# Kernel optimization log

Measured on AMD Instinct MI355X. Metric: run time of the kernel, lower is better.

Reference implementation:

```python
import jax, jax.numpy as jnp
import numpy as np

N_NODES = 50000
N_EDGES = 800000
D_IN, D_HID, D_OUT = 128, 128, 64


def setup_inputs() -> dict:
    key = jax.random.key(0)
    ks = jax.random.split(key, 8)
    x = jax.random.normal(ks[0], (N_NODES, D_IN), dtype=jnp.float32)
    edge_index = jax.random.randint(ks[1], (2, N_EDGES), 0, N_NODES, dtype=jnp.int64)

    def glorot(k, shape):
        fan_in, fan_out = shape
        lim = jnp.sqrt(6.0 / (fan_in + fan_out)).astype(jnp.float32)
        return jax.random.uniform(k, shape, jnp.float32, -lim, lim)

    return {
        "x": x,
        "edge_index": edge_index,
        "W1": glorot(ks[2], (D_IN, D_HID)),
        "b1": jnp.zeros((D_HID,), jnp.float32),
        "W2": glorot(ks[3], (D_HID, D_HID)),
        "b2": jnp.zeros((D_HID,), jnp.float32),
        "W3": glorot(ks[4], (D_HID, D_OUT)),
        "b3": jnp.zeros((D_OUT,), jnp.float32),
    }


def reference(x, edge_index, W1, b1, W2, b2, W3, b3):
    # PyG GCNConv with normalize=False: h = x @ W, then sum-aggregate source
    # features onto targets (edge_index[0]=src, edge_index[1]=dst), add bias.
    src = edge_index[0]
    dst = edge_index[1]
    n = x.shape[0]

    def gcn_layer(h, W, b):
        hw = h @ W                      # [N, d_out] dense GEMM
        msg = hw[src]                   # [E, d_out] gather
        agg = jax.ops.segment_sum(msg, dst, num_segments=n)  # [N, d_out] scatter-add
        return agg + b

    o1 = gcn_layer(x, W1, b1)
    o2 = gcn_layer(o1, W2, b2)
    o3 = gcn_layer(o2, W3, b3)
    return (o1, o2, o3)
```

## Files before the change

kernel.cpp:

```cpp
#include <hip/hip_runtime.h>

#define N_NODES 50000
#define N_EDGES 800000
#define CAP 64

typedef unsigned int uint32;
typedef unsigned short u16;

typedef __attribute__((ext_vector_type(8))) short bf16x8;
typedef __attribute__((ext_vector_type(4))) float f32x4;

__device__ __forceinline__ uint32 f32_to_bf16_rne(float f) {
    uint32 u = __float_as_uint(f);
    u += 0x7fffu + ((u >> 16) & 1u);
    return u >> 16;
}
__device__ __forceinline__ float bf16lo_to_f32(uint32 v) { return __uint_as_float(v << 16); }
__device__ __forceinline__ float bf16hi_to_f32(uint32 v) { return __uint_as_float(v & 0xffff0000u); }

__global__ __launch_bounds__(256) void prep_kernel(const float* __restrict__ W1,
                                                   const float* __restrict__ W2,
                                                   const float* __restrict__ W3,
                                                   uint32* __restrict__ wt1,
                                                   uint32* __restrict__ wt2,
                                                   uint32* __restrict__ wt3,
                                                   int* __restrict__ cursor) {
    int b = blockIdx.x, tid = threadIdx.x;
    if (b < 196) {
        int i = b * 256 + tid;
        if (i < N_NODES) cursor[i] = 0;
        return;
    }
    b -= 196;
    const float* W;
    uint32* WT;
    int N;
    if (b < 32) { W = W1; WT = wt1; N = 128; }
    else if (b < 64) { W = W2; WT = wt2; N = 128; b -= 32; }
    else { W = W3; WT = wt3; N = 64; b -= 64; }
    int i = b * 256 + tid;
    if (i >= N * 64) return;
    int n = i >> 6, p = i & 63;
    WT[n * 64 + p] = f32_to_bf16_rne(W[(2 * p) * N + n]) |
                     (f32_to_bf16_rne(W[(2 * p + 1) * N + n]) << 16);
}

__device__ __forceinline__ void gather_pair(const uint32* __restrict__ hwb,
                                            int myslot, int d, int lane,
                                            float& ax, float& ay, float& az, float& aw) {
    const int h = lane >> 5;
    const int li = lane & 31;
    int e = 0;
    for (; e + 16 <= d; e += 16) {
        uint2 v[8];
#pragma unroll
        for (int j = 0; j < 8; j++) {
            int s = __shfl(myslot, e + 2 * j + h);
            v[j] = *reinterpret_cast<const uint2*>(&hwb[(size_t)s * 64 + li * 2]);
        }
#pragma unroll
        for (int j = 0; j < 8; j++) {
            ax += bf16lo_to_f32(v[j].x); ay += bf16hi_to_f32(v[j].x);
            az += bf16lo_to_f32(v[j].y); aw += bf16hi_to_f32(v[j].y);
        }
    }
    for (; e < d; e += 2) {
        int idx = e + h;
        int s = __shfl(myslot, idx < d ? idx : e);
        uint2 v = make_uint2(0u, 0u);
        if (idx < d) v = *reinterpret_cast<const uint2*>(&hwb[(size_t)s * 64 + li * 2]);
        ax += bf16lo_to_f32(v.x); ay += bf16hi_to_f32(v.x);
        az += bf16lo_to_f32(v.y); aw += bf16hi_to_f32(v.y);
    }
    ax += __shfl_xor(ax, 32);
    ay += __shfl_xor(ay, 32);
    az += __shfl_xor(az, 32);
    aw += __shfl_xor(aw, 32);
}

__device__ __forceinline__ void pack_store(uint32* __restrict__ Cb, int rowstride_u,
                                           int row, int col, int r16, float v) {
    float nb = __shfl_xor(v, 1);
    if ((r16 & 1) == 0) {
        uint32 p = f32_to_bf16_rne(v) | (f32_to_bf16_rne(nb) << 16);
        Cb[(size_t)row * rowstride_u + (col >> 1)] = p;
    }
}

__device__ __forceinline__ void gemm1_body(const float* __restrict__ A,
                                           const uint32* __restrict__ WTb,
                                           uint32* __restrict__ Cb, int M, int bid) {
    constexpr int NT = 2;
    const int tid = threadIdx.x;
    const int wave = tid >> 6;
    const int lane = tid & 63;
    const int r16 = lane & 15;
    const int g = lane >> 4;
    const int row0 = bid * 64;

    const float4* A4 = reinterpret_cast<const float4*>(A);
    const uint4* B4 = reinterpret_cast<const uint4*>(WTb);

    f32x4 acc[4][NT];
#pragma unroll
    for (int m = 0; m < 4; m++)
#pragma unroll
        for (int nt = 0; nt < NT; nt++) acc[m][nt] = (f32x4){0.f, 0.f, 0.f, 0.f};

    int rowm[4];
#pragma unroll
    for (int m = 0; m < 4; m++) {
        int r = row0 + m * 16 + r16;
        rowm[m] = r < M ? r : M - 1;
    }
    union U { uint4 u; bf16x8 v; };
#pragma unroll
    for (int kt = 0; kt < 4; kt++) {
        U b[NT];
#pragma unroll
        for (int nt = 0; nt < NT; nt++)
            b[nt].u = B4[(size_t)(nt * 64 + wave * 16 + r16) * 16 + kt * 4 + g];
        U a[4];
#pragma unroll
        for (int m = 0; m < 4; m++) {
            float4 f0 = A4[(size_t)rowm[m] * 32 + kt * 8 + g * 2];
            float4 f1 = A4[(size_t)rowm[m] * 32 + kt * 8 + g * 2 + 1];
            a[m].u.x = f32_to_bf16_rne(f0.x) | (f32_to_bf16_rne(f0.y) << 16);
            a[m].u.y = f32_to_bf16_rne(f0.z) | (f32_to_bf16_rne(f0.w) << 16);
            a[m].u.z = f32_to_bf16_rne(f1.x) | (f32_to_bf16_rne(f1.y) << 16);
            a[m].u.w = f32_to_bf16_rne(f1.z) | (f32_to_bf16_rne(f1.w) << 16);
        }
#pragma unroll
        for (int m = 0; m < 4; m++)
#pragma unroll
            for (int nt = 0; nt < NT; nt++)
                acc[m][nt] = __builtin_amdgcn_mfma_f32_16x16x32_bf16(a[m].v, b[nt].v, acc[m][nt], 0, 0, 0);
    }
#pragma unroll
    for (int m = 0; m < 4; m++)
#pragma unroll
        for (int nt = 0; nt < NT; nt++)
#pragma unroll
            for (int r = 0; r < 4; r++) {
                int row = row0 + m * 16 + g * 4 + r;
                if (row < M)
                    pack_store(Cb, 64, row, nt * 64 + wave * 16 + r16, r16, acc[m][nt][r]);
            }
}

#define EPT 8
#define EPB (256 * EPT)
#define GEMM1_BLOCKS 782
#define BUILD_CHUNKS 391

__global__ __launch_bounds__(256) void build_gemm1_kernel(const float* __restrict__ x,
                                                          const uint32* __restrict__ wt1,
                                                          uint32* __restrict__ hwb,
                                                          const int* __restrict__ ei,
                                                          int* __restrict__ cursor,
                                                          u16* __restrict__ adj) {
    if (blockIdx.x < GEMM1_BLOCKS) {
        gemm1_body(x, wt1, hwb, N_NODES, blockIdx.x);
        return;
    }
    const int bb = blockIdx.x - GEMM1_BLOCKS;
    const int part = bb & 7;
    const int chunk = bb >> 3;
    const int base = chunk * EPB + threadIdx.x * EPT;
#pragma unroll
    for (int i = 0; i < EPT; i += 4) {
        int e = base + i;
        if (e + 3 < N_EDGES) {
            int4 s4 = *reinterpret_cast<const int4*>(&ei[e]);
            int4 d4 = *reinterpret_cast<const int4*>(&ei[N_EDGES + e]);
            int ss[4] = {s4.x, s4.y, s4.z, s4.w};
            int dd[4] = {d4.x, d4.y, d4.z, d4.w};
#pragma unroll
            for (int j = 0; j < 4; j++) {
                int d = dd[j];
                if (((d >> 4) & 7) == part && (unsigned)d < (unsigned)N_NODES) {
                    int s = ss[j];
                    if ((unsigned)s >= (unsigned)N_NODES) s = 0;
                    int pos = atomicAdd(&cursor[d], 1);
                    if (pos < CAP) adj[d * CAP + pos] = (u16)s;
                }
            }
        } else {
            for (int j = 0; j < 4; j++) {
                int ee = e + j;
                if (ee < N_EDGES) {
                    int d = ei[N_EDGES + ee];
                    if (((d >> 4) & 7) == part && (unsigned)d < (unsigned)N_NODES) {
                        int s = ei[ee];
                        if ((unsigned)s >= (unsigned)N_NODES) s = 0;
                        int pos = atomicAdd(&cursor[d], 1);
                        if (pos < CAP) adj[d * CAP + pos] = (u16)s;
                    }
                }
            }
        }
    }
}

template <int N>
__global__ __launch_bounds__(256) void agg_gemm_kernel(const uint32* __restrict__ hw_in,
                                                       const u16* __restrict__ adj,
                                                       const int* __restrict__ deg,
                                                       const float* __restrict__ bias,
                                                       float* __restrict__ o_out,
                                                       const uint32* __restrict__ WTb,
                                                       uint32* __restrict__ hw_out) {
    constexpr int TPW = N / 64;
    constexpr int LDR = 68;
    __shared__ uint32 Asm[16 * LDR];

    const int tid = threadIdx.x;
    const int wave = tid >> 6;
    const int lane = tid & 63;
    const int li = lane & 31;
    const int base = blockIdx.x * 16;
    const float4* bias4 = reinterpret_cast<const float4*>(bias);

#pragma unroll
    for (int i = 0; i < 4; i++) {
        int n = base + wave * 4 + i;
        int d = __builtin_amdgcn_readfirstlane(deg[n]);
        if (d > CAP) d = CAP;
        int myslot = adj[n * CAP + lane];
        float ax = 0.f, ay = 0.f, az = 0.f, aw = 0.f;
        gather_pair(hw_in, myslot, d, lane, ax, ay, az, aw);
        if (lane < 32) {
            float4 b = bias4[li];
            ax += b.x; ay += b.y; az += b.z; aw += b.w;
            *reinterpret_cast<float4*>(&o_out[(size_t)n * 128 + li * 4]) =
                make_float4(ax, ay, az, aw);
            uint2 p;
            p.x = f32_to_bf16_rne(ax) | (f32_to_bf16_rne(ay) << 16);
            p.y = f32_to_bf16_rne(az) | (f32_to_bf16_rne(aw) << 16);
            *reinterpret_cast<uint2*>(&Asm[(wave * 4 + i) * LDR + li * 2]) = p;
        }
    }
    __syncthreads();

    const int r16 = lane & 15;
    const int g = lane >> 4;
    const uint4* B4 = reinterpret_cast<const uint4*>(WTb);

    f32x4 acc[TPW];
#pragma unroll
    for (int nt = 0; nt < TPW; nt++) acc[nt] = (f32x4){0.f, 0.f, 0.f, 0.f};

    union U { uint4 u; bf16x8 v; };
#pragma unroll
    for (int kt = 0; kt < 4; kt++) {
        U a;
        a.u = *reinterpret_cast<const uint4*>(&Asm[r16 * LDR + (kt * 4 + g) * 4]);
        U b[TPW];
#pragma unroll
        for (int nt = 0; nt < TPW; nt++) {
            int col = (wave * TPW + nt) * 16 + r16;
            b[nt].u = B4[(size_t)col * 16 + kt * 4 + g];
        }
#pragma unroll
        for (int nt = 0; nt < TPW; nt++)
            acc[nt] = __builtin_amdgcn_mfma_f32_16x16x32_bf16(a.v, b[nt].v, acc[nt], 0, 0, 0);
    }
#pragma unroll
    for (int nt = 0; nt < TPW; nt++)
#pragma unroll
        for (int r = 0; r < 4; r++) {
            int row = base + g * 4 + r;
            pack_store(hw_out, N / 2, row, (wave * TPW + nt) * 16 + r16, r16, acc[nt][r]);
        }
}

__global__ __launch_bounds__(256) void aggregate64_kernel(const uint32* __restrict__ hwb,
                                                          const u16* __restrict__ adj,
                                                          const int* __restrict__ deg,
                                                          const float* __restrict__ bias,
                                                          float* __restrict__ out) {
    int n = (blockIdx.x * blockDim.x + threadIdx.x) >> 6;
    if (n >= N_NODES) return;
    const int lane = threadIdx.x & 63;
    const int q = lane >> 4;
    const int li = lane & 15;
    int d = __builtin_amdgcn_readfirstlane(deg[n]);
    if (d > CAP) d = CAP;
    int myslot = adj[n * CAP + lane];

    float ax = 0.f, ay = 0.f, az = 0.f, aw = 0.f;
    int e = 0;
    for (; e + 32 <= d; e += 32) {
        uint2 v[8];
#pragma unroll
        for (int j = 0; j < 8; j++) {
            int s = __shfl(myslot, e + 4 * j + q);
            v[j] = *reinterpret_cast<const uint2*>(&hwb[(size_t)s * 32 + li * 2]);
        }
#pragma unroll
        for (int j = 0; j < 8; j++) {
            ax += bf16lo_to_f32(v[j].x); ay += bf16hi_to_f32(v[j].x);
            az += bf16lo_to_f32(v[j].y); aw += bf16hi_to_f32(v[j].y);
        }
    }
    for (; e < d; e += 4) {
        int idx = e + q;
        int s = __shfl(myslot, idx < d ? idx : e);
        uint2 v = make_uint2(0u, 0u);
        if (idx < d) v = *reinterpret_cast<const uint2*>(&hwb[(size_t)s * 32 + li * 2]);
        ax += bf16lo_to_f32(v.x); ay += bf16hi_to_f32(v.x);
        az += bf16lo_to_f32(v.y); aw += bf16hi_to_f32(v.y);
    }
    ax += __shfl_xor(ax, 32); ay += __shfl_xor(ay, 32);
    az += __shfl_xor(az, 32); aw += __shfl_xor(aw, 32);
    ax += __shfl_xor(ax, 16); ay += __shfl_xor(ay, 16);
    az += __shfl_xor(az, 16); aw += __shfl_xor(aw, 16);
    if (lane < 16) {
        const float4* bias4 = reinterpret_cast<const float4*>(bias);
        float4 b = bias4[li];
        *reinterpret_cast<float4*>(&out[(size_t)n * 64 + li * 4]) =
            make_float4(ax + b.x, ay + b.y, az + b.z, aw + b.w);
    }
}

extern "C" void kernel_launch(void* const* d_in, const int* in_sizes, int n_in,
                              void* d_out, int out_size, void* d_ws, size_t ws_size,
                              hipStream_t stream) {
    const float* x  = (const float*)d_in[0];
    const int*   ei = (const int*)d_in[1];
    const float* W1 = (const float*)d_in[2];
    const float* b1 = (const float*)d_in[3];
    const float* W2 = (const float*)d_in[4];
    const float* b2 = (const float*)d_in[5];
    const float* W3 = (const float*)d_in[6];
    const float* b3 = (const float*)d_in[7];

    float* o1 = (float*)d_out;
    float* o2 = o1 + (size_t)N_NODES * 128;
    float* o3 = o2 + (size_t)N_NODES * 128;

    char* ws = (char*)d_ws;
    uint32* hwbA   = (uint32*)(ws);
    uint32* hwbB   = (uint32*)(ws + 12800000);
    u16*    adj    = (u16*)(ws + 25600000);
    int*    cursor = (int*)(ws + 32000000);
    uint32* wt1    = (uint32*)(ws + 32200000);
    uint32* wt2    = (uint32*)(ws + 32232768);
    uint32* wt3    = (uint32*)(ws + 32265536);

    prep_kernel<<<276, 256, 0, stream>>>(W1, W2, W3, wt1, wt2, wt3, cursor);
    build_gemm1_kernel<<<GEMM1_BLOCKS + BUILD_CHUNKS * 8, 256, 0, stream>>>(x, wt1, hwbA, ei, cursor, adj);
    agg_gemm_kernel<128><<<3125, 256, 0, stream>>>(hwbA, adj, cursor, b1, o1, wt2, hwbB);
    agg_gemm_kernel<64><<<3125, 256, 0, stream>>>(hwbB, adj, cursor, b2, o2, wt3, hwbA);
    aggregate64_kernel<<<12500, 256, 0, stream>>>(hwbA, adj, cursor, b3, o3);
}
```

Before: 175.5 us.

## Split fused aggregate-GEMM into feature-sliced aggregation plus standalone MFMA GEMM

Replaces the fused aggregate+GEMM kernels with separate passes: a feature-sliced aggregation kernel, where each block gathers one quarter of the feature columns for 16 nodes, followed by a standalone bf16 MFMA GEMM over 64-row tiles. Slicing the features shrinks the set of rows being randomly gathered at any moment, so neighbour reads should hit in cache more often. The cost is two extra kernel launches and extra round trips of intermediate bf16 activations through global memory. The second-layer GEMM also runs in place on its input buffer.

Result: slower. 247.3 us (+41.0%).

```diff
diff --git a/kernel.cpp b/kernel.cpp
--- a/kernel.cpp
+++ b/kernel.cpp
@@ -45,39 +45,6 @@
                      (f32_to_bf16_rne(W[(2 * p + 1) * N + n]) << 16);
 }
 
-__device__ __forceinline__ void gather_pair(const uint32* __restrict__ hwb,
-                                            int myslot, int d, int lane,
-                                            float& ax, float& ay, float& az, float& aw) {
-    const int h = lane >> 5;
-    const int li = lane & 31;
-    int e = 0;
-    for (; e + 16 <= d; e += 16) {
-        uint2 v[8];
-#pragma unroll
-        for (int j = 0; j < 8; j++) {
-            int s = __shfl(myslot, e + 2 * j + h);
-            v[j] = *reinterpret_cast<const uint2*>(&hwb[(size_t)s * 64 + li * 2]);
-        }
-#pragma unroll
-        for (int j = 0; j < 8; j++) {
-            ax += bf16lo_to_f32(v[j].x); ay += bf16hi_to_f32(v[j].x);
-            az += bf16lo_to_f32(v[j].y); aw += bf16hi_to_f32(v[j].y);
-        }
-    }
-    for (; e < d; e += 2) {
-        int idx = e + h;
-        int s = __shfl(myslot, idx < d ? idx : e);
-        uint2 v = make_uint2(0u, 0u);
-        if (idx < d) v = *reinterpret_cast<const uint2*>(&hwb[(size_t)s * 64 + li * 2]);
-        ax += bf16lo_to_f32(v.x); ay += bf16hi_to_f32(v.x);
-        az += bf16lo_to_f32(v.y); aw += bf16hi_to_f32(v.y);
-    }
-    ax += __shfl_xor(ax, 32);
-    ay += __shfl_xor(ay, 32);
-    az += __shfl_xor(az, 32);
-    aw += __shfl_xor(aw, 32);
-}
-
 __device__ __forceinline__ void pack_store(uint32* __restrict__ Cb, int rowstride_u,
                                            int row, int col, int r16, float v) {
     float nb = __shfl_xor(v, 1);
@@ -203,123 +170,134 @@
 }
 
 template <int N>
-__global__ __launch_bounds__(256) void agg_gemm_kernel(const uint32* __restrict__ hw_in,
-                                                       const u16* __restrict__ adj,
-                                                       const int* __restrict__ deg,
-                                                       const float* __restrict__ bias,
-                                                       float* __restrict__ o_out,
-                                                       const uint32* __restrict__ WTb,
-                                                       uint32* __restrict__ hw_out) {
-    constexpr int TPW = N / 64;
-    constexpr int LDR = 68;
-    __shared__ uint32 Asm[16 * LDR];
-
+__global__ __launch_bounds__(256) void mfma_gemm_kernel(const uint32* __restrict__ Ab,
+                                                        const uint32* __restrict__ WTb,
+                                                        uint32* __restrict__ Cb, int M) {
+    constexpr int NT = N / 64;
     const int tid = threadIdx.x;
     const int wave = tid >> 6;
     const int lane = tid & 63;
-    const int li = lane & 31;
-    const int base = blockIdx.x * 16;
-    const float4* bias4 = reinterpret_cast<const float4*>(bias);
+    const int r16 = lane & 15;
+    const int g = lane >> 4;
+    const int row0 = blockIdx.x * 64;
+
+    const uint4* A4 = reinterpret_cast<const uint4*>(Ab);
+    const uint4* B4 = reinterpret_cast<const uint4*>(WTb);
+
+    f32x4 acc[4][NT];
+#pragma unroll
+    for (int m = 0; m < 4; m++)
+#pragma unroll
+        for (int nt = 0; nt < NT; nt++) acc[m][nt] = (f32x4){0.f, 0.f, 0.f, 0.f};
+
+    int rowm[4];
+#pragma unroll
+    for (int m = 0; m < 4; m++) {
+        int r = row0 + m * 16 + r16;
+        rowm[m] = r < M ? r : M - 1;
+    }
+    union U { uint4 u; bf16x8 v; };
+#pragma unroll
+    for (int kt = 0; kt < 4; kt++) {
+        U b[NT];
+#pragma unroll
+        for (int nt = 0; nt < NT; nt++)
+            b[nt].u = B4[(size_t)(nt * 64 + wave * 16 + r16) * 16 + kt * 4 + g];
+        U a[4];
+#pragma unroll
+        for (int m = 0; m < 4; m++) a[m].u = A4[(size_t)rowm[m] * 16 + kt * 4 + g];
+#pragma unroll
+        for (int m = 0; m < 4; m++)
+#pragma unroll
+            for (int nt = 0; nt < NT; nt++)
+                acc[m][nt] = __builtin_amdgcn_mfma_f32_16x16x32_bf16(a[m].v, b[nt].v, acc[m][nt], 0, 0, 0);
+    }
+    __syncthreads();
+#pragma unroll
+    for (int m = 0; m < 4; m++)
+#pragma unroll
+        for (int nt = 0; nt < NT; nt++)
+#pragma unroll
+            for (int r = 0; r < 4; r++) {
+                int row = row0 + m * 16 + g * 4 + r;
+                if (row < M)
+                    pack_store(Cb, N / 2, row, nt * 64 + wave * 16 + r16, r16, acc[m][nt][r]);
+            }
+}
+
+template <int F, bool WRITE_BF>
+__global__ __launch_bounds__(256) void agg_slice_kernel(const uint32* __restrict__ hwb,
+                                                        const u16* __restrict__ adj,
+                                                        const int* __restrict__ deg,
+                                                        const float* __restrict__ bias,
+                                                        float* __restrict__ o_out,
+                                                        uint32* __restrict__ obf) {
+    constexpr int ROWU = F / 2;
+    constexpr int SU = ROWU / 4;
+    constexpr int L = SU / 2;
+    constexpr int E = 64 / L;
+
+    const int x = blockIdx.x & 7;
+    const int g = blockIdx.x >> 3;
+    const int slice = x >> 1;
+    const int h = x & 1;
+    const int wave = threadIdx.x >> 6;
+    const int lane = threadIdx.x & 63;
+    const int f = lane % L;
+    const int j = lane / L;
+
+    const int nbase = g * 32 + h * 16 + wave * 4;
+    const uint32* sbase = hwb + slice * SU + f * 2;
 
 #pragma unroll
     for (int i = 0; i < 4; i++) {
-        int n = base + wave * 4 + i;
+        int n = nbase + i;
+        if (n >= N_NODES) return;
         int d = __builtin_amdgcn_readfirstlane(deg[n]);
         if (d > CAP) d = CAP;
         int myslot = adj[n * CAP + lane];
-        float ax = 0.f, ay = 0.f, az = 0.f, aw = 0.f;
-        gather_pair(hw_in, myslot, d, lane, ax, ay, az, aw);
-        if (lane < 32) {
-            float4 b = bias4[li];
-            ax += b.x; ay += b.y; az += b.z; aw += b.w;
-            *reinterpret_cast<float4*>(&o_out[(size_t)n * 128 + li * 4]) =
-                make_float4(ax, ay, az, aw);
-            uint2 p;
-            p.x = f32_to_bf16_rne(ax) | (f32_to_bf16_rne(ay) << 16);
-            p.y = f32_to_bf16_rne(az) | (f32_to_bf16_rne(aw) << 16);
-            *reinterpret_cast<uint2*>(&Asm[(wave * 4 + i) * LDR + li * 2]) = p;
-        }
-    }
-    __syncthreads();
-
-    const int r16 = lane & 15;
-    const int g = lane >> 4;
-    const uint4* B4 = reinterpret_cast<const uint4*>(WTb);
-
-    f32x4 acc[TPW];
-#pragma unroll
-    for (int nt = 0; nt < TPW; nt++) acc[nt] = (f32x4){0.f, 0.f, 0.f, 0.f};
-
-    union U { uint4 u; bf16x8 v; };
-#pragma unroll
-    for (int kt = 0; kt < 4; kt++) {
-        U a;
-        a.u = *reinterpret_cast<const uint4*>(&Asm[r16 * LDR + (kt * 4 + g) * 4]);
-        U b[TPW];
-#pragma unroll
-        for (int nt = 0; nt < TPW; nt++) {
-            int col = (wave * TPW + nt) * 16 + r16;
-            b[nt].u = B4[(size_t)col * 16 + kt * 4 + g];
-        }
-#pragma unroll
-        for (int nt = 0; nt < TPW; nt++)
-            acc[nt] = __builtin_amdgcn_mfma_f32_16x16x32_bf16(a.v, b[nt].v, acc[nt], 0, 0, 0);
-    }
-#pragma unroll
-    for (int nt = 0; nt < TPW; nt++)
-#pragma unroll
-        for (int r = 0; r < 4; r++) {
-            int row = base + g * 4 + r;
-            pack_store(hw_out, N / 2, row, (wave * TPW + nt) * 16 + r16, r16, acc[nt][r]);
-        }
-}
-
-__global__ __launch_bounds__(256) void aggregate64_kernel(const uint32* __restrict__ hwb,
-                                                          const u16* __restrict__ adj,
-                                                          const int* __restrict__ deg,
-                                                          const float* __restrict__ bias,
-                                                          float* __restrict__ out) {
-    int n = (blockIdx.x * blockDim.x + threadIdx.x) >> 6;
-    if (n >= N_NODES) return;
-    const int lane = threadIdx.x & 63;
-    const int q = lane >> 4;
-    const int li = lane & 15;
-    int d = __builtin_amdgcn_readfirstlane(deg[n]);
-    if (d > CAP) d = CAP;
-    int myslot = adj[n * CAP + lane];
-
-    float ax = 0.f, ay = 0.f, az = 0.f, aw = 0.f;
-    int e = 0;
-    for (; e + 32 <= d; e += 32) {
-        uint2 v[8];
-#pragma unroll
-        for (int j = 0; j < 8; j++) {
-            int s = __shfl(myslot, e + 4 * j + q);
-            v[j] = *reinterpret_cast<const uint2*>(&hwb[(size_t)s * 32 + li * 2]);
-        }
-#pragma unroll
-        for (int j = 0; j < 8; j++) {
-            ax += bf16lo_to_f32(v[j].x); ay += bf16hi_to_f32(v[j].x);
-            az += bf16lo_to_f32(v[j].y); aw += bf16hi_to_f32(v[j].y);
-        }
-    }
-    for (; e < d; e += 4) {
-        int idx = e + q;
-        int s = __shfl(myslot, idx < d ? idx : e);
-        uint2 v = make_uint2(0u, 0u);
-        if (idx < d) v = *reinterpret_cast<const uint2*>(&hwb[(size_t)s * 32 + li * 2]);
-        ax += bf16lo_to_f32(v.x); ay += bf16hi_to_f32(v.x);
-        az += bf16lo_to_f32(v.y); aw += bf16hi_to_f32(v.y);
-    }
-    ax += __shfl_xor(ax, 32); ay += __shfl_xor(ay, 32);
-    az += __shfl_xor(az, 32); aw += __shfl_xor(aw, 32);
-    ax += __shfl_xor(ax, 16); ay += __shfl_xor(ay, 16);
-    az += __shfl_xor(az, 16); aw += __shfl_xor(aw, 16);
-    if (lane < 16) {
-        const float4* bias4 = reinterpret_cast<const float4*>(bias);
-        float4 b = bias4[li];
-        *reinterpret_cast<float4*>(&out[(size_t)n * 64 + li * 4]) =
-            make_float4(ax + b.x, ay + b.y, az + b.z, aw + b.w);
+
+        float a0 = 0.f, a1 = 0.f, a2 = 0.f, a3 = 0.f;
+        int e = 0;
+        for (; e + 2 * E <= d; e += 2 * E) {
+            int s0 = __shfl(myslot, e + j);
+            int s1 = __shfl(myslot, e + E + j);
+            uint2 v0 = *reinterpret_cast<const uint2*>(sbase + (size_t)s0 * ROWU);
+            uint2 v1 = *reinterpret_cast<const uint2*>(sbase + (size_t)s1 * ROWU);
+            a0 += bf16lo_to_f32(v0.x) + bf16lo_to_f32(v1.x);
+            a1 += bf16hi_to_f32(v0.x) + bf16hi_to_f32(v1.x);
+            a2 += bf16lo_to_f32(v0.y) + bf16lo_to_f32(v1.y);
+            a3 += bf16hi_to_f32(v0.y) + bf16hi_to_f32(v1.y);
+        }
+        for (; e < d; e += E) {
+            int idx = e + j;
+            int s = __shfl(myslot, idx < d ? idx : e);
+            uint2 v = make_uint2(0u, 0u);
+            if (idx < d) v = *reinterpret_cast<const uint2*>(sbase + (size_t)s * ROWU);
+            a0 += bf16lo_to_f32(v.x);
+            a1 += bf16hi_to_f32(v.x);
+            a2 += bf16lo_to_f32(v.y);
+            a3 += bf16hi_to_f32(v.y);
+        }
+#pragma unroll
+        for (int off = L; off < 64; off <<= 1) {
+            a0 += __shfl_xor(a0, off);
+            a1 += __shfl_xor(a1, off);
+            a2 += __shfl_xor(a2, off);
+            a3 += __shfl_xor(a3, off);
+        }
+        if (lane < L) {
+            float4 b = *reinterpret_cast<const float4*>(&bias[slice * SU * 2 + f * 4]);
+            a0 += b.x; a1 += b.y; a2 += b.z; a3 += b.w;
+            *reinterpret_cast<float4*>(&o_out[(size_t)n * F + slice * SU * 2 + f * 4]) =
+                make_float4(a0, a1, a2, a3);
+            if (WRITE_BF) {
+                uint2 p;
+                p.x = f32_to_bf16_rne(a0) | (f32_to_bf16_rne(a1) << 16);
+                p.y = f32_to_bf16_rne(a2) | (f32_to_bf16_rne(a3) << 16);
+                *reinterpret_cast<uint2*>(&obf[(size_t)n * ROWU + slice * SU + f * 2]) = p;
+            }
+        }
     }
 }
 
@@ -340,17 +318,22 @@
     float* o3 = o2 + (size_t)N_NODES * 128;
 
     char* ws = (char*)d_ws;
-    uint32* hwbA   = (uint32*)(ws);
-    uint32* hwbB   = (uint32*)(ws + 12800000);
-    u16*    adj    = (u16*)(ws + 25600000);
-    int*    cursor = (int*)(ws + 32000000);
-    uint32* wt1    = (uint32*)(ws + 32200000);
-    uint32* wt2    = (uint32*)(ws + 32232768);
-    uint32* wt3    = (uint32*)(ws + 32265536);
+    uint32* bufA   = (uint32*)(ws);
+    uint32* bufB   = (uint32*)(ws + 12800000);
+    uint32* bufC   = (uint32*)(ws + 25600000);
+    u16*    adj    = (u16*)(ws + 32000000);
+    int*    cursor = (int*)(ws + 38400000);
+    uint32* wt1    = (uint32*)(ws + 38600000);
+    uint32* wt2    = (uint32*)(ws + 38632768);
+    uint32* wt3    = (uint32*)(ws + 38665536);
+
+    const int agg_grid = 1563 * 8;
 
     prep_kernel<<<276, 256, 0, stream>>>(W1, W2, W3, wt1, wt2, wt3, cursor);
-    build_gemm1_kernel<<<GEMM1_BLOCKS + BUILD_CHUNKS * 8, 256, 0, stream>>>(x, wt1, hwbA, ei, cursor, adj);
-    agg_gemm_kernel<128><<<3125, 256, 0, stream>>>(hwbA, adj, cursor, b1, o1, wt2, hwbB);
-    agg_gemm_kernel<64><<<3125, 256, 0, stream>>>(hwbB, adj, cursor, b2, o2, wt3, hwbA);
-    aggregate64_kernel<<<12500, 256, 0, stream>>>(hwbA, adj, cursor, b3, o3);
-}
+    build_gemm1_kernel<<<GEMM1_BLOCKS + BUILD_CHUNKS * 8, 256, 0, stream>>>(x, wt1, bufA, ei, cursor, adj);
+    agg_slice_kernel<128, true><<<agg_grid, 256, 0, stream>>>(bufA, adj, cursor, b1, o1, bufB);
+    mfma_gemm_kernel<128><<<GEMM1_BLOCKS, 256, 0, stream>>>(bufB, wt2, bufB, N_NODES);
+    agg_slice_kernel<128, true><<<agg_grid, 256, 0, stream>>>(bufB, adj, cursor, b2, o2, bufA);
+    mfma_gemm_kernel<64><<<GEMM1_BLOCKS, 256, 0, stream>>>(bufA, wt3, bufC, N_NODES);
+    agg_slice_kernel<64, false><<<agg_grid, 256, 0, stream>>>(bufC, adj, cursor, b3, o3, nullptr);
+}
```
